# Kernel tuning notes

Hardware: AMD Instinct MI355X
Metric: run time of the kernel (lower is better)

The kernel has to match this reference:

```python
import jax, jax.numpy as jnp
import numpy as np

B, C, H, N = 4, 128, 4, 2048
D = C // H  # head_dim = 32
BN_EPS = 1e-5


def _conv1(w, b, x):
    # 1x1 Conv1d: [O,C] x [B,C,N] -> [B,O,N]
    return jnp.einsum('oc,bcn->bon', w, x) + b[None, :, None]


def setup_inputs() -> dict:
    key = jax.random.key(0)
    ks = jax.random.split(key, 20)
    p = lambda k, shape: jax.random.normal(k, shape, dtype=jnp.float32) * 0.05
    return {
        'x1': jax.random.normal(ks[0], (B, C, N), dtype=jnp.float32),
        'x2': jax.random.normal(ks[1], (B, C, N), dtype=jnp.float32),
        'kv_mask': jnp.ones((B, N), dtype=bool),
        'wq': p(ks[2], (C, C)), 'bq': p(ks[3], (C,)),
        'wk': p(ks[4], (C, C)), 'bk': p(ks[5], (C,)),
        'wv': p(ks[6], (C, C)), 'bv': p(ks[7], (C,)),
        'wm': p(ks[8], (C, C)), 'bm': p(ks[9], (C,)),
        'wc1': p(ks[10], (2 * C, 2 * C)), 'bc1': p(ks[11], (2 * C,)),
        'bn_gamma': jnp.ones((2 * C,), dtype=jnp.float32),
        'bn_beta': jnp.zeros((2 * C,), dtype=jnp.float32),
        'bn_mean': p(ks[12], (2 * C,)),
        'bn_var': jax.random.uniform(ks[13], (2 * C,), dtype=jnp.float32, minval=0.5, maxval=1.5),
        'wc2': p(ks[14], (C, 2 * C)), 'bc2': p(ks[15], (C,)),
    }


def reference(x1, x2, kv_mask, wq, bq, wk, bk, wv, bv, wm, bm,
              wc1, bc1, bn_gamma, bn_beta, bn_mean, bn_var, wc2, bc2):
    b, _, n = x1.shape
    q = _conv1(wq, bq, x1).reshape(b, H, D, n)   # bhdn
    k = _conv1(wk, bk, x2).reshape(b, H, D, -1)  # bhdm
    v = _conv1(wv, bv, x2).reshape(b, H, D, -1)  # bhdm
    qk = jnp.einsum('bhdn,bhdm->bhnm', q, k)
    # masked_fill on raw QK before scaling, matching torch code
    qk = jnp.where(kv_mask[:, None, None, :], qk, jnp.float32(-1e6))
    score = jax.nn.softmax(qk * (1.0 / D ** 0.5), axis=-1)
    add_value = jnp.einsum('bhnm,bhdm->bhdn', score, v).reshape(b, C, n)
    add_value = _conv1(wm, bm, add_value)
    cat = jnp.concatenate([x1, add_value], axis=1)  # [B, 2C, N]
    h = _conv1(wc1, bc1, cat)
    # BatchNorm1d in inference mode (running stats)
    h = (h - bn_mean[None, :, None]) * jax.lax.rsqrt(bn_var[None, :, None] + BN_EPS)
    h = h * bn_gamma[None, :, None] + bn_beta[None, :, None]
    h = jax.nn.relu(h)
    h = _conv1(wc2, bc2, h)
    return x1 + h
```

## Files before the change

kernel.cpp:

```cpp
#include <hip/hip_runtime.h>

typedef __attribute__((ext_vector_type(4))) float v4f;
typedef __attribute__((ext_vector_type(8))) _Float16 half8;
typedef __attribute__((ext_vector_type(4))) _Float16 half4;
typedef __attribute__((ext_vector_type(2))) _Float16 half2t;

constexpr float C2 = 0.17677669529663687f * 1.44269504088896341f;

__device__ __forceinline__ half4 pk4(float a, float b, float c, float d) {
  half2t lo = __builtin_bit_cast(half2t, __builtin_amdgcn_cvt_pkrtz(a, b));
  half2t hi = __builtin_bit_cast(half2t, __builtin_amdgcn_cvt_pkrtz(c, d));
  return __builtin_shufflevector(lo, hi, 0, 1, 2, 3);
}
__device__ __forceinline__ half8 pk8f4(const float4 a, const float4 b) {
  const half4 lo = pk4(a.x, a.y, a.z, a.w);
  const half4 hi = pk4(b.x, b.y, b.z, b.w);
  return __builtin_shufflevector(lo, hi, 0, 1, 2, 3, 4, 5, 6, 7);
}

__global__ __launch_bounds__(512, 4) void qkv(
    const float* __restrict__ x1, const float* __restrict__ x2,
    const float* __restrict__ wq, const float* __restrict__ bq,
    const float* __restrict__ wk, const float* __restrict__ bk,
    const float* __restrict__ wv, const float* __restrict__ bv,
    const float* __restrict__ wm, const float* __restrict__ wc1,
    const float* __restrict__ wc2, const unsigned char* __restrict__ mask,
    _Float16* __restrict__ Qpk, _Float16* __restrict__ Kpk,
    _Float16* __restrict__ Vpk, _Float16* __restrict__ wts,
    float* __restrict__ maskf) {
  const int b = blockIdx.y;
  const int bx = blockIdx.x;
  const int tid = threadIdx.x, w = tid >> 6, lane = tid & 63;
  const int l = lane & 15, q = lane >> 4;
  const int n0 = bx * 32;

  __shared__ _Float16 x1s[2][16 * 136];
  __shared__ _Float16 x2s[2][16 * 136];

  if (b == 0) {
    const int e = (bx * 512 + tid) * 4;
    const float* src;
    int base;
    if (e < 16384) { src = wm; base = 0; }
    else if (e < 81920) { src = wc1; base = 16384; }
    else { src = wc2; base = 81920; }
    const float4 t = *(const float4*)(src + (e - base));
    *(half4*)(wts + e) = pk4(t.x, t.y, t.z, t.w);
  } else if (b == 1 && bx < 8) {
    const int e = (((64 + bx) * 512) + tid) * 4;
    const float* src;
    int base;
    if (e < 81920) { src = wc1; base = 16384; }
    else { src = wc2; base = 81920; }
    const float4 t = *(const float4*)(src + (e - base));
    *(half4*)(wts + e) = pk4(t.x, t.y, t.z, t.w);
  } else if (b == 2 && bx < 4) {
    const int e = (bx * 512 + tid) * 4;
    const unsigned mv = *(const unsigned*)(mask + e);
    float4 o;
    o.x = (mv & 0x000000ffu) ? 0.f : -1.0e6f * C2;
    o.y = (mv & 0x0000ff00u) ? 0.f : -1.0e6f * C2;
    o.z = (mv & 0x00ff0000u) ? 0.f : -1.0e6f * C2;
    o.w = (mv & 0xff000000u) ? 0.f : -1.0e6f * C2;
    *(float4*)(maskf + e) = o;
  }

  {
    const int ch = tid >> 2, seg = tid & 3;
#pragma unroll
    for (int g = 0; g < 2; ++g) {
      const float4 a =
          *(const float4*)(x1 + (size_t)(b * 128 + ch) * 2048 + n0 + g * 16 + seg * 4);
      const float4 c =
          *(const float4*)(x2 + (size_t)(b * 128 + ch) * 2048 + n0 + g * 16 + seg * 4);
      x1s[g][(seg * 4 + 0) * 136 + ch] = (_Float16)a.x;
      x1s[g][(seg * 4 + 1) * 136 + ch] = (_Float16)a.y;
      x1s[g][(seg * 4 + 2) * 136 + ch] = (_Float16)a.z;
      x1s[g][(seg * 4 + 3) * 136 + ch] = (_Float16)a.w;
      x2s[g][(seg * 4 + 0) * 136 + ch] = (_Float16)c.x;
      x2s[g][(seg * 4 + 1) * 136 + ch] = (_Float16)c.y;
      x2s[g][(seg * 4 + 2) * 136 + ch] = (_Float16)c.z;
      x2s[g][(seg * 4 + 3) * 136 + ch] = (_Float16)c.w;
    }
  }
  __syncthreads();

#pragma unroll
  for (int i = 0; i < 3; ++i) {
    const int t = w * 3 + i;
    if (t < 8) {
      const int mt = t;
      half8 wf[4];
#pragma unroll
      for (int kt = 0; kt < 4; ++kt) {
        const float4 wa = *(const float4*)(wq + (mt * 16 + l) * 128 + kt * 32 + q * 8);
        const float4 wb = *(const float4*)(wq + (mt * 16 + l) * 128 + kt * 32 + q * 8 + 4);
        wf[kt] = pk8f4(wa, wb);
      }
      const v4f bias = *(const v4f*)(bq + mt * 16 + q * 4);
#pragma unroll
      for (int g = 0; g < 2; ++g) {
        v4f acc = bias;
#pragma unroll
        for (int kt = 0; kt < 4; ++kt) {
          const half8 xf = *(const half8*)&x1s[g][l * 136 + kt * 32 + q * 8];
          acc = __builtin_amdgcn_mfma_f32_16x16x32_f16(wf[kt], xf, acc, 0, 0, 0);
        }
        *(half4*)(Qpk + ((size_t)(b * 8 + mt) * 2048 + n0 + g * 16 + l) * 16 + q * 4) =
            pk4(acc[0] * C2, acc[1] * C2, acc[2] * C2, acc[3] * C2);
      }
    } else if (t < 16) {
      const int mt = t - 8;
      half8 wf[4];
#pragma unroll
      for (int kt = 0; kt < 4; ++kt) {
        const float4 wa = *(const float4*)(wk + (mt * 16 + l) * 128 + kt * 32 + q * 8);
        const float4 wb = *(const float4*)(wk + (mt * 16 + l) * 128 + kt * 32 + q * 8 + 4);
        wf[kt] = pk8f4(wa, wb);
      }
      const v4f bias = *(const v4f*)(bk + mt * 16 + q * 4);
#pragma unroll
      for (int g = 0; g < 2; ++g) {
        v4f acc = bias;
#pragma unroll
        for (int kt = 0; kt < 4; ++kt) {
          const half8 xf = *(const half8*)&x2s[g][l * 136 + kt * 32 + q * 8];
          acc = __builtin_amdgcn_mfma_f32_16x16x32_f16(wf[kt], xf, acc, 0, 0, 0);
        }
        *(half4*)(Kpk + ((size_t)(b * 8 + mt) * 2048 + n0 + g * 16 + l) * 16 + q * 4) =
            pk4(acc[0], acc[1], acc[2], acc[3]);
      }
    } else {
      const int ot = t - 16;
      half8 wf[4];
#pragma unroll
      for (int kt = 0; kt < 4; ++kt) {
        const float4 wa = *(const float4*)(wv + (ot * 16 + l) * 128 + kt * 32 + q * 8);
        const float4 wb = *(const float4*)(wv + (ot * 16 + l) * 128 + kt * 32 + q * 8 + 4);
        wf[kt] = pk8f4(wa, wb);
      }
      const float bvv = bv[ot * 16 + l];
#pragma unroll
      for (int g = 0; g < 2; ++g) {
        v4f acc = {bvv, bvv, bvv, bvv};
#pragma unroll
        for (int kt = 0; kt < 4; ++kt) {
          const half8 xf = *(const half8*)&x2s[g][l * 136 + kt * 32 + q * 8];
          acc = __builtin_amdgcn_mfma_f32_16x16x32_f16(xf, wf[kt], acc, 0, 0, 0);
        }
        const int kx = bx * 2 + g;
        *(half4*)(Vpk + (((size_t)(b * 4 + (ot >> 1)) * 128 + kx) * 32 +
                         (ot & 1) * 16 + l) * 16 + q * 4) =
            pk4(acc[0], acc[1], acc[2], acc[3]);
      }
    }
  }
}

__global__ __launch_bounds__(256) void attn(
    const _Float16* __restrict__ Qpk, const _Float16* __restrict__ Kpk,
    const _Float16* __restrict__ Vpk, const float* __restrict__ maskf,
    _Float16* __restrict__ Opk, float* __restrict__ lsump) {
  const int bh = blockIdx.y, b = bh >> 2, h = bh & 3;
  const int part = blockIdx.z;
  const int tid = threadIdx.x, w = tid >> 6, lane = tid & 63;
  const int l = lane & 15, q = lane >> 4;
  const int nb = blockIdx.x * 128 + w * 32;

  __shared__ _Float16 ldsK[2][3088];
  __shared__ _Float16 ldsV[2][3072];
  __shared__ __align__(16) float biass[512];

  const size_t qrow = (size_t)(b * 8 + h * 2 + (q >> 1)) * 2048;
  const half8 qf0 = *(const half8*)(Qpk + (qrow + nb + l) * 16 + (q & 1) * 8);
  const half8 qf1 = *(const half8*)(Qpk + (qrow + nb + 16 + l) * 16 + (q & 1) * 8);
  const _Float16* __restrict__ Kg = Kpk + (size_t)(b * 8 + h * 2) * 2048 * 16;
  const _Float16* __restrict__ Vg = Vpk + (size_t)((b * 4 + h) * 128) * 512;

  const int kct = tid >> 7, kk = (tid >> 1) & 63, khf = tid & 1;
  const int vt = tid >> 6, vd = (tid >> 1) & 31;

  v4f oacc[2][2] = {{{0.f, 0.f, 0.f, 0.f}, {0.f, 0.f, 0.f, 0.f}},
                    {{0.f, 0.f, 0.f, 0.f}, {0.f, 0.f, 0.f, 0.f}}};
  v4f lsacc[2] = {{0.f, 0.f, 0.f, 0.f}, {0.f, 0.f, 0.f, 0.f}};
  const half4 ones = {(_Float16)1.f, (_Float16)1.f, (_Float16)1.f, (_Float16)1.f};
  const int mbeg = part * 512;

  if (tid < 128)
    *(float4*)&biass[tid * 4] = *(const float4*)(maskf + b * 2048 + mbeg + tid * 4);
  half8 kr = *(const half8*)(Kg + ((size_t)kct * 2048 + mbeg + kk) * 16 + khf * 8);
  half8 vr = *(const half8*)(Vg + (size_t)((mbeg >> 4) + vt) * 512 + vd * 16 + khf * 8);
  *(half8*)&ldsK[0][kct * 1544 + kk * 24 + khf * 8] = kr;
  *(half8*)&ldsV[0][vt * 768 + vd * 24 + khf * 8] = vr;
  __syncthreads();

  for (int i = 0; i < 8; ++i) {
    const int m0 = mbeg + i * 64;
    const int cur = i & 1;
    if (i < 7) {
      kr = *(const half8*)(Kg + ((size_t)kct * 2048 + m0 + 64 + kk) * 16 + khf * 8);
      vr = *(const half8*)(Vg + (size_t)(((m0 + 64) >> 4) + vt) * 512 + vd * 16 + khf * 8);
    }
    half4 pB[2][4];
#pragma unroll
    for (int mt = 0; mt < 4; ++mt) {
      const half8 kf =
          *(const half8*)&ldsK[cur][(q >> 1) * 1544 + (mt * 16 + l) * 24 + (q & 1) * 8];
      const v4f biasv = *(const v4f*)&biass[i * 64 + mt * 16 + q * 4];
      __builtin_amdgcn_s_setprio(1);
      const v4f s0 = __builtin_amdgcn_mfma_f32_16x16x32_f16(kf, qf0, biasv, 0, 0, 0);
      const v4f s1 = __builtin_amdgcn_mfma_f32_16x16x32_f16(kf, qf1, biasv, 0, 0, 0);
      __builtin_amdgcn_s_setprio(0);
      const float a0 = exp2f(s0[0]), a1 = exp2f(s0[1]), a2 = exp2f(s0[2]),
                  a3 = exp2f(s0[3]);
      const float c0 = exp2f(s1[0]), c1 = exp2f(s1[1]), c2 = exp2f(s1[2]),
                  c3 = exp2f(s1[3]);
      pB[0][mt] = pk4(a0, a1, a2, a3);
      pB[1][mt] = pk4(c0, c1, c2, c3);
    }
    __builtin_amdgcn_s_setprio(1);
#pragma unroll
    for (int mt = 0; mt < 4; ++mt) {
      const half4 vf0 = *(const half4*)&ldsV[cur][mt * 768 + l * 24 + q * 4];
      const half4 vf1 = *(const half4*)&ldsV[cur][mt * 768 + (16 + l) * 24 + q * 4];
      oacc[0][0] = __builtin_amdgcn_mfma_f32_16x16x16f16(vf0, pB[0][mt], oacc[0][0], 0, 0, 0);
      oacc[0][1] = __builtin_amdgcn_mfma_f32_16x16x16f16(vf1, pB[0][mt], oacc[0][1], 0, 0, 0);
      oacc[1][0] = __builtin_amdgcn_mfma_f32_16x16x16f16(vf0, pB[1][mt], oacc[1][0], 0, 0, 0);
      oacc[1][1] = __builtin_amdgcn_mfma_f32_16x16x16f16(vf1, pB[1][mt], oacc[1][1], 0, 0, 0);
      lsacc[0] = __builtin_amdgcn_mfma_f32_16x16x16f16(ones, pB[0][mt], lsacc[0], 0, 0, 0);
      lsacc[1] = __builtin_amdgcn_mfma_f32_16x16x16f16(ones, pB[1][mt], lsacc[1], 0, 0, 0);
    }
    __builtin_amdgcn_s_setprio(0);
    if (i < 7) {
      *(half8*)&ldsK[cur ^ 1][kct * 1544 + kk * 24 + khf * 8] = kr;
      *(half8*)&ldsV[cur ^ 1][vt * 768 + vd * 24 + khf * 8] = vr;
      __syncthreads();
    }
  }
  if (q == 0) {
    lsump[part * 32768 + bh * 2048 + nb + l] = lsacc[0][0];
    lsump[part * 32768 + bh * 2048 + nb + 16 + l] = lsacc[1][0];
  }
#pragma unroll
  for (int qt = 0; qt < 2; ++qt)
#pragma unroll
    for (int df = 0; df < 2; ++df)
      *(half4*)(Opk + (size_t)part * 1048576 +
                ((size_t)(b * 8 + h * 2 + df) * 2048 + nb + qt * 16 + l) * 16 +
                q * 4) = pk4(oacc[qt][df][0], oacc[qt][df][1], oacc[qt][df][2],
                             oacc[qt][df][3]);
}

__global__ __launch_bounds__(512, 4) void post(
    const float* __restrict__ x1, const _Float16* __restrict__ Opk,
    const float* __restrict__ lsump, const _Float16* __restrict__ wts,
    const float* __restrict__ bm, const float* __restrict__ bc1,
    const float* __restrict__ gamma, const float* __restrict__ beta,
    const float* __restrict__ mean, const float* __restrict__ var,
    const float* __restrict__ bc2, float* __restrict__ out) {
  const int b = blockIdx.y;
  const int n0 = blockIdx.x * 32;
  const int tid = threadIdx.x, w = tid >> 6, lane = tid & 63;
  const int l = lane & 15, q = lane >> 4;
  const _Float16* wm_h = wts;
  const _Float16* wc1_h = wts + 16384;
  const _Float16* wc2_h = wts + 81920;

  __shared__ __align__(16) float x1s[2][16 * 132];
  __shared__ __align__(16) _Float16 x1h[2][8 * 256];
  __shared__ __align__(16) _Float16 ofs[2][8 * 256];
  __shared__ __align__(16) _Float16 exA[2][8 * 256];
  __shared__ __align__(16) _Float16 exB[2][16 * 256];

  {
    const int ch = tid >> 2, seg = tid & 3;
#pragma unroll
    for (int g = 0; g < 2; ++g) {
      const float4 a =
          *(const float4*)(x1 + (size_t)(b * 128 + ch) * 2048 + n0 + g * 16 + seg * 4);
      x1s[g][(seg * 4 + 0) * 132 + ch] = a.x;
      x1s[g][(seg * 4 + 1) * 132 + ch] = a.y;
      x1s[g][(seg * 4 + 2) * 132 + ch] = a.z;
      x1s[g][(seg * 4 + 3) * 132 + ch] = a.w;
    }
  }
  {
#pragma unroll
    for (int g = 0; g < 2; ++g) {
      const int n = n0 + g * 16 + l;
      const size_t idx = (size_t)(b * 4 + (w >> 1)) * 2048 + n;
      const float rl = 1.0f / (lsump[idx] + lsump[32768 + idx] +
                               lsump[65536 + idx] + lsump[98304 + idx]);
      const size_t oa = ((size_t)(b * 8 + w) * 2048 + n) * 16 + q * 4;
      const half4 a = *(const half4*)(Opk + oa);
      const half4 c = *(const half4*)(Opk + 1048576 + oa);
      const half4 d = *(const half4*)(Opk + 2097152 + oa);
      const half4 e = *(const half4*)(Opk + 3145728 + oa);
      const _Float16 rh = (_Float16)rl;
      const half4 rl4 = {rh, rh, rh, rh};
      *(half4*)&ofs[g][w * 256 + l * 16 + q * 4] = ((a + c) + (d + e)) * rl4;
    }
  }
  __syncthreads();
  {
#pragma unroll
    for (int g = 0; g < 2; ++g) {
      const float4 xv = *(const float4*)&x1s[g][l * 132 + w * 16 + q * 4];
      *(half4*)&x1h[g][w * 256 + l * 16 + q * 4] = pk4(xv.x, xv.y, xv.z, xv.w);
    }
  }
  __syncthreads();

  {
    const v4f bias = *(const v4f*)(bm + w * 16 + q * 4);
    v4f acc[2] = {bias, bias};
#pragma unroll
    for (int kt = 0; kt < 8; ++kt) {
      const half4 wf = *(const half4*)(wm_h + (w * 16 + l) * 128 + kt * 16 + q * 4);
#pragma unroll
      for (int g = 0; g < 2; ++g) {
        const half4 of = *(const half4*)&ofs[g][kt * 256 + l * 16 + q * 4];
        acc[g] = __builtin_amdgcn_mfma_f32_16x16x16f16(wf, of, acc[g], 0, 0, 0);
      }
    }
#pragma unroll
    for (int g = 0; g < 2; ++g)
      *(half4*)&exA[g][w * 256 + l * 16 + q * 4] =
          pk4(acc[g][0], acc[g][1], acc[g][2], acc[g][3]);
  }
  __syncthreads();
#pragma unroll
  for (int i = 0; i < 2; ++i) {
    const int mt = w * 2 + i;
    const v4f bias = *(const v4f*)(bc1 + mt * 16 + q * 4);
    v4f acc[2] = {bias, bias};
#pragma unroll
    for (int kt = 0; kt < 16; ++kt) {
      const half4 wf = *(const half4*)(wc1_h + (mt * 16 + l) * 256 + kt * 16 + q * 4);
#pragma unroll
      for (int g = 0; g < 2; ++g) {
        const half4 frag =
            (kt < 8) ? *(const half4*)&x1h[g][kt * 256 + l * 16 + q * 4]
                     : *(const half4*)&exA[g][(kt - 8) * 256 + l * 16 + q * 4];
        acc[g] = __builtin_amdgcn_mfma_f32_16x16x16f16(wf, frag, acc[g], 0, 0, 0);
      }
    }
    const v4f gm = *(const v4f*)(gamma + mt * 16 + q * 4);
    const v4f bt = *(const v4f*)(beta + mt * 16 + q * 4);
    const v4f mn = *(const v4f*)(mean + mt * 16 + q * 4);
    const v4f vr = *(const v4f*)(var + mt * 16 + q * 4);
#pragma unroll
    for (int g = 0; g < 2; ++g) {
      float hh[4];
#pragma unroll
      for (int r = 0; r < 4; ++r) {
        const float a1 = gm[r] * rsqrtf(vr[r] + 1e-5f);
        const float b1 = bt[r] - mn[r] * a1;
        hh[r] = fmaxf(acc[g][r] * a1 + b1, 0.f);
      }
      *(half4*)&exB[g][mt * 256 + l * 16 + q * 4] = pk4(hh[0], hh[1], hh[2], hh[3]);
    }
  }
  __syncthreads();
  {
    const v4f bias = *(const v4f*)(bc2 + w * 16 + q * 4);
    v4f acc[2] = {bias, bias};
#pragma unroll
    for (int kt = 0; kt < 16; ++kt) {
      const half4 wf = *(const half4*)(wc2_h + (w * 16 + l) * 256 + kt * 16 + q * 4);
#pragma unroll
      for (int g = 0; g < 2; ++g) {
        const half4 hfv = *(const half4*)&exB[g][kt * 256 + l * 16 + q * 4];
        acc[g] = __builtin_amdgcn_mfma_f32_16x16x16f16(wf, hfv, acc[g], 0, 0, 0);
      }
    }
#pragma unroll
    for (int g = 0; g < 2; ++g) {
      const int n = n0 + g * 16 + l;
#pragma unroll
      for (int r = 0; r < 4; ++r)
        out[(size_t)(b * 128 + w * 16 + q * 4 + r) * 2048 + n] =
            acc[g][r] + x1s[g][l * 132 + w * 16 + q * 4 + r];
    }
  }
}

extern "C" void kernel_launch(void* const* d_in, const int* in_sizes, int n_in,
                              void* d_out, int out_size, void* d_ws,
                              size_t ws_size, hipStream_t stream) {
  const float* x1 = (const float*)d_in[0];
  const float* x2 = (const float*)d_in[1];
  const unsigned char* kv_mask = (const unsigned char*)d_in[2];
  const float* wq = (const float*)d_in[3];
  const float* bq = (const float*)d_in[4];
  const float* wk = (const float*)d_in[5];
  const float* bk = (const float*)d_in[6];
  const float* wv = (const float*)d_in[7];
  const float* bv = (const float*)d_in[8];
  const float* wm = (const float*)d_in[9];
  const float* bm = (const float*)d_in[10];
  const float* wc1 = (const float*)d_in[11];
  const float* bc1 = (const float*)d_in[12];
  const float* bn_gamma = (const float*)d_in[13];
  const float* bn_beta = (const float*)d_in[14];
  const float* bn_mean = (const float*)d_in[15];
  const float* bn_var = (const float*)d_in[16];
  const float* wc2 = (const float*)d_in[17];
  const float* bc2 = (const float*)d_in[18];
  float* out = (float*)d_out;

  char* p = (char*)d_ws;
  _Float16* Qpk = (_Float16*)p;
  _Float16* Kpk = (_Float16*)(p + (size_t)2 * 1024 * 1024);
  _Float16* Vpk = (_Float16*)(p + (size_t)4 * 1024 * 1024);
  _Float16* Opk = (_Float16*)(p + (size_t)6 * 1024 * 1024);
  _Float16* wts = (_Float16*)(p + (size_t)14 * 1024 * 1024);
  float* lsump = (float*)(p + (size_t)14 * 1024 * 1024 + 512 * 1024);
  float* maskf = lsump + 4 * 32768;

  qkv<<<dim3(64, 4), 512, 0, stream>>>(x1, x2, wq, bq, wk, bk, wv, bv, wm,
                                       wc1, wc2, kv_mask, Qpk, Kpk, Vpk, wts,
                                       maskf);
  attn<<<dim3(16, 16, 4), 256, 0, stream>>>(Qpk, Kpk, Vpk, maskf, Opk, lsump);
  post<<<dim3(64, 4), 512, 0, stream>>>(x1, Opk, lsump, wts, bm, bc1,
                                        bn_gamma, bn_beta, bn_mean, bn_var,
                                        bc2, out);
}
```

Measured before the change: 143.1 us.

## Split weight and mask conversion into a separate prep kernel; merge post concat buffers

```diff
diff --git a/kernel.cpp b/kernel.cpp
--- a/kernel.cpp
+++ b/kernel.cpp
@@ -12,58 +12,60 @@
   half2t hi = __builtin_bit_cast(half2t, __builtin_amdgcn_cvt_pkrtz(c, d));
   return __builtin_shufflevector(lo, hi, 0, 1, 2, 3);
 }
-__device__ __forceinline__ half8 pk8f4(const float4 a, const float4 b) {
-  const half4 lo = pk4(a.x, a.y, a.z, a.w);
-  const half4 hi = pk4(b.x, b.y, b.z, b.w);
-  return __builtin_shufflevector(lo, hi, 0, 1, 2, 3, 4, 5, 6, 7);
+
+__global__ __launch_bounds__(512) void prep(
+    const float* __restrict__ wq, const float* __restrict__ wk,
+    const float* __restrict__ wv, const float* __restrict__ wm,
+    const float* __restrict__ wc1, const float* __restrict__ wc2,
+    const unsigned char* __restrict__ mask, _Float16* __restrict__ wqkvh,
+    _Float16* __restrict__ wts, float* __restrict__ maskf) {
+  const int e = (blockIdx.x * 512 + threadIdx.x) * 4;
+  if (e < 49152) {
+    const float* src;
+    int base;
+    if (e < 16384) { src = wq; base = 0; }
+    else if (e < 32768) { src = wk; base = 16384; }
+    else { src = wv; base = 32768; }
+    const float4 t = *(const float4*)(src + (e - base));
+    *(half4*)(wqkvh + e) = pk4(t.x, t.y, t.z, t.w);
+  } else if (e < 196608) {
+    const int e2 = e - 49152;
+    const float* src;
+    int base;
+    if (e2 < 16384) { src = wm; base = 0; }
+    else if (e2 < 81920) { src = wc1; base = 16384; }
+    else { src = wc2; base = 81920; }
+    const float4 t = *(const float4*)(src + (e2 - base));
+    *(half4*)(wts + e2) = pk4(t.x, t.y, t.z, t.w);
+  } else {
+    const int e2 = e - 196608;
+    const unsigned mv = *(const unsigned*)(mask + e2);
+    float4 o;
+    o.x = (mv & 0x000000ffu) ? 0.f : -1.0e6f * C2;
+    o.y = (mv & 0x0000ff00u) ? 0.f : -1.0e6f * C2;
+    o.z = (mv & 0x00ff0000u) ? 0.f : -1.0e6f * C2;
+    o.w = (mv & 0xff000000u) ? 0.f : -1.0e6f * C2;
+    *(float4*)(maskf + e2) = o;
+  }
 }
 
 __global__ __launch_bounds__(512, 4) void qkv(
     const float* __restrict__ x1, const float* __restrict__ x2,
-    const float* __restrict__ wq, const float* __restrict__ bq,
-    const float* __restrict__ wk, const float* __restrict__ bk,
-    const float* __restrict__ wv, const float* __restrict__ bv,
-    const float* __restrict__ wm, const float* __restrict__ wc1,
-    const float* __restrict__ wc2, const unsigned char* __restrict__ mask,
+    const _Float16* __restrict__ wqkvh, const float* __restrict__ bq,
+    const float* __restrict__ bk, const float* __restrict__ bv,
     _Float16* __restrict__ Qpk, _Float16* __restrict__ Kpk,
-    _Float16* __restrict__ Vpk, _Float16* __restrict__ wts,
-    float* __restrict__ maskf) {
+    _Float16* __restrict__ Vpk) {
   const int b = blockIdx.y;
   const int bx = blockIdx.x;
   const int tid = threadIdx.x, w = tid >> 6, lane = tid & 63;
   const int l = lane & 15, q = lane >> 4;
   const int n0 = bx * 32;
+  const _Float16* wqh = wqkvh;
+  const _Float16* wkh = wqkvh + 16384;
+  const _Float16* wvh = wqkvh + 32768;
 
   __shared__ _Float16 x1s[2][16 * 136];
   __shared__ _Float16 x2s[2][16 * 136];
-
-  if (b == 0) {
-    const int e = (bx * 512 + tid) * 4;
-    const float* src;
-    int base;
-    if (e < 16384) { src = wm; base = 0; }
-    else if (e < 81920) { src = wc1; base = 16384; }
-    else { src = wc2; base = 81920; }
-    const float4 t = *(const float4*)(src + (e - base));
-    *(half4*)(wts + e) = pk4(t.x, t.y, t.z, t.w);
-  } else if (b == 1 && bx < 8) {
-    const int e = (((64 + bx) * 512) + tid) * 4;
-    const float* src;
-    int base;
-    if (e < 81920) { src = wc1; base = 16384; }
-    else { src = wc2; base = 81920; }
-    const float4 t = *(const float4*)(src + (e - base));
-    *(half4*)(wts + e) = pk4(t.x, t.y, t.z, t.w);
-  } else if (b == 2 && bx < 4) {
-    const int e = (bx * 512 + tid) * 4;
-    const unsigned mv = *(const unsigned*)(mask + e);
-    float4 o;
-    o.x = (mv & 0x000000ffu) ? 0.f : -1.0e6f * C2;
-    o.y = (mv & 0x0000ff00u) ? 0.f : -1.0e6f * C2;
-    o.z = (mv & 0x00ff0000u) ? 0.f : -1.0e6f * C2;
-    o.w = (mv & 0xff000000u) ? 0.f : -1.0e6f * C2;
-    *(float4*)(maskf + e) = o;
-  }
 
   {
     const int ch = tid >> 2, seg = tid & 3;
@@ -92,11 +94,8 @@
       const int mt = t;
       half8 wf[4];
 #pragma unroll
-      for (int kt = 0; kt < 4; ++kt) {
-        const float4 wa = *(const float4*)(wq + (mt * 16 + l) * 128 + kt * 32 + q * 8);
-        const float4 wb = *(const float4*)(wq + (mt * 16 + l) * 128 + kt * 32 + q * 8 + 4);
-        wf[kt] = pk8f4(wa, wb);
-      }
+      for (int kt = 0; kt < 4; ++kt)
+        wf[kt] = *(const half8*)(wqh + (mt * 16 + l) * 128 + kt * 32 + q * 8);
       const v4f bias = *(const v4f*)(bq + mt * 16 + q * 4);
 #pragma unroll
       for (int g = 0; g < 2; ++g) {
@@ -113,11 +112,8 @@
       const int mt = t - 8;
       half8 wf[4];
 #pragma unroll
-      for (int kt = 0; kt < 4; ++kt) {
-        const float4 wa = *(const float4*)(wk + (mt * 16 + l) * 128 + kt * 32 + q * 8);
-        const float4 wb = *(const float4*)(wk + (mt * 16 + l) * 128 + kt * 32 + q * 8 + 4);
-        wf[kt] = pk8f4(wa, wb);
-      }
+      for (int kt = 0; kt < 4; ++kt)
+        wf[kt] = *(const half8*)(wkh + (mt * 16 + l) * 128 + kt * 32 + q * 8);
       const v4f bias = *(const v4f*)(bk + mt * 16 + q * 4);
 #pragma unroll
       for (int g = 0; g < 2; ++g) {
@@ -134,11 +130,8 @@
       const int ot = t - 16;
       half8 wf[4];
 #pragma unroll
-      for (int kt = 0; kt < 4; ++kt) {
-        const float4 wa = *(const float4*)(wv + (ot * 16 + l) * 128 + kt * 32 + q * 8);
-        const float4 wb = *(const float4*)(wv + (ot * 16 + l) * 128 + kt * 32 + q * 8 + 4);
-        wf[kt] = pk8f4(wa, wb);
-      }
+      for (int kt = 0; kt < 4; ++kt)
+        wf[kt] = *(const half8*)(wvh + (ot * 16 + l) * 128 + kt * 32 + q * 8);
       const float bvv = bv[ot * 16 + l];
 #pragma unroll
       for (int g = 0; g < 2; ++g) {
@@ -267,9 +260,8 @@
   const _Float16* wc2_h = wts + 81920;
 
   __shared__ __align__(16) float x1s[2][16 * 132];
-  __shared__ __align__(16) _Float16 x1h[2][8 * 256];
   __shared__ __align__(16) _Float16 ofs[2][8 * 256];
-  __shared__ __align__(16) _Float16 exA[2][8 * 256];
+  __shared__ __align__(16) _Float16 catl[2][16 * 256];
   __shared__ __align__(16) _Float16 exB[2][16 * 256];
 
   {
@@ -306,11 +298,9 @@
 #pragma unroll
     for (int g = 0; g < 2; ++g) {
       const float4 xv = *(const float4*)&x1s[g][l * 132 + w * 16 + q * 4];
-      *(half4*)&x1h[g][w * 256 + l * 16 + q * 4] = pk4(xv.x, xv.y, xv.z, xv.w);
-    }
-  }
-  __syncthreads();
-
+      *(half4*)&catl[g][w * 256 + l * 16 + q * 4] = pk4(xv.x, xv.y, xv.z, xv.w);
+    }
+  }
   {
     const v4f bias = *(const v4f*)(bm + w * 16 + q * 4);
     v4f acc[2] = {bias, bias};
@@ -325,7 +315,7 @@
     }
 #pragma unroll
     for (int g = 0; g < 2; ++g)
-      *(half4*)&exA[g][w * 256 + l * 16 + q * 4] =
+      *(half4*)&catl[g][(8 + w) * 256 + l * 16 + q * 4] =
           pk4(acc[g][0], acc[g][1], acc[g][2], acc[g][3]);
   }
   __syncthreads();
@@ -339,9 +329,7 @@
       const half4 wf = *(const half4*)(wc1_h + (mt * 16 + l) * 256 + kt * 16 + q * 4);
 #pragma unroll
       for (int g = 0; g < 2; ++g) {
-        const half4 frag =
-            (kt < 8) ? *(const half4*)&x1h[g][kt * 256 + l * 16 + q * 4]
-                     : *(const half4*)&exA[g][(kt - 8) * 256 + l * 16 + q * 4];
+        const half4 frag = *(const half4*)&catl[g][kt * 256 + l * 16 + q * 4];
         acc[g] = __builtin_amdgcn_mfma_f32_16x16x16f16(wf, frag, acc[g], 0, 0, 0);
       }
     }
@@ -416,11 +404,13 @@
   _Float16* Opk = (_Float16*)(p + (size_t)6 * 1024 * 1024);
   _Float16* wts = (_Float16*)(p + (size_t)14 * 1024 * 1024);
   float* lsump = (float*)(p + (size_t)14 * 1024 * 1024 + 512 * 1024);
-  float* maskf = lsump + 4 * 32768;
-
-  qkv<<<dim3(64, 4), 512, 0, stream>>>(x1, x2, wq, bq, wk, bk, wv, bv, wm,
-                                       wc1, wc2, kv_mask, Qpk, Kpk, Vpk, wts,
-                                       maskf);
+  float* maskf = (float*)(p + (size_t)15 * 1024 * 1024);
+  _Float16* wqkvh = (_Float16*)(p + (size_t)15 * 1024 * 1024 + 64 * 1024);
+
+  prep<<<dim3(100), 512, 0, stream>>>(wq, wk, wv, wm, wc1, wc2, kv_mask,
+                                      wqkvh, wts, maskf);
+  qkv<<<dim3(64, 4), 512, 0, stream>>>(x1, x2, wqkvh, bq, bk, bv, Qpk, Kpk,
+                                       Vpk);
   attn<<<dim3(16, 16, 4), 256, 0, stream>>>(Qpk, Kpk, Vpk, maskf, Opk, lsump);
   post<<<dim3(64, 4), 512, 0, stream>>>(x1, Opk, lsump, wts, bm, bc1,
                                         bn_gamma, bn_beta, bn_mean, bn_var,
```

Result: no change. 142.5 us (-0.4%).
